# Kernel tuning notes

Measured on AMD Instinct MI355X. Metric: run time of the kernel, lower is better.

## Reference

```python
import jax, jax.numpy as jnp
import numpy as np

NH = 12
RD = 16  # partial RoPE dim


def setup_inputs() -> dict:
    key = jax.random.key(0)
    k1, k2, k3 = jax.random.split(key, 3)
    B, T, C = 4, 2048, 768
    x = jax.random.normal(k1, (B, T, C), dtype=jnp.float32)
    w_qkv = jax.random.normal(k2, (3 * C, C), dtype=jnp.float32) * 0.02
    w_out = jax.random.normal(k3, (C, C), dtype=jnp.float32) * 0.02
    return {"x": x, "w_qkv": w_qkv, "w_out": w_out}


def _rope_tables(T, dtype):
    freqs = 1.0 / (10000.0 ** (jnp.arange(0, RD, 2, dtype=jnp.float32) / RD))
    f = jnp.arange(T, dtype=jnp.float32)[:, None] * freqs[None, :]  # [T, RD//2]
    cos = jnp.cos(f)[None, None].astype(dtype)  # [1,1,T,RD//2]
    sin = jnp.sin(f)[None, None].astype(dtype)
    return cos, sin


def _rope(t, cos, sin):
    # t: [B, H, T, hd]; rotate only the first RD dims (split-half style)
    r, p = t[..., :RD], t[..., RD:]
    r1, r2 = r[..., : RD // 2], r[..., RD // 2 :]
    rot = jnp.concatenate([r1 * cos - r2 * sin, r2 * cos + r1 * sin], axis=-1)
    return jnp.concatenate([rot, p], axis=-1)


def reference(x, w_qkv, w_out):
    B, T, C = x.shape
    hd = C // NH
    qkv = jnp.einsum('btc,dc->btd', x, w_qkv).reshape(B, T, 3, NH, hd)
    q, k, v = (jnp.transpose(qkv[:, :, i], (0, 2, 1, 3)) for i in range(3))  # [B,H,T,hd]
    cos, sin = _rope_tables(T, x.dtype)
    q = _rope(q, cos, sin)
    k = _rope(k, cos, sin)
    scale = 1.0 / np.sqrt(hd).astype(np.float32)
    scores = jnp.einsum('bhqd,bhkd->bhqk', q, k) * scale  # [B,H,T,T]
    causal = jnp.tril(jnp.ones((T, T), dtype=bool))
    scores = jnp.where(causal[None, None], scores, jnp.finfo(scores.dtype).min)
    attn = jax.nn.softmax(scores, axis=-1)
    o = jnp.einsum('bhqk,bhkd->bhqd', attn, v)  # [B,H,T,hd]
    o = jnp.transpose(o, (0, 2, 1, 3)).reshape(B, T, C)
    return jnp.einsum('btc,dc->btd', o, w_out)
```

## Files before the change

kernel.cpp:

```cpp
#include <hip/hip_runtime.h>
#include <math.h>


namespace {

constexpr int B_ = 4, T_ = 2048, C_ = 768, NH_ = 12, HD_ = 64;
constexpr int BH_ = B_ * NH_;
constexpr size_t QS_ = (size_t)BH_ * T_ * HD_;

typedef short short8 __attribute__((ext_vector_type(8)));
typedef float f32x4 __attribute__((ext_vector_type(4)));

__device__ inline ushort f2bf(float f) {
    unsigned u = __builtin_bit_cast(unsigned, f);
    u += 0x7fff + ((u >> 16) & 1);
    return (ushort)(u >> 16);
}
__device__ inline float bf2f(ushort h) {
    unsigned u = (unsigned)h << 16;
    return __builtin_bit_cast(float, u);
}

__global__ __launch_bounds__(256) void cvt_all(
    const float4* __restrict__ x, const float4* __restrict__ wq,
    const float4* __restrict__ wo, ushort4* __restrict__ xb,
    ushort4* __restrict__ wqb, ushort4* __restrict__ wob)
{
    int i = blockIdx.x * 256 + threadIdx.x;
    const float4* s; ushort4* d;
    if (i < 1572864) { s = x; d = xb; }
    else if (i < 2015232) { s = wq; d = wqb; i -= 1572864; }
    else { s = wo; d = wob; i -= 2015232; if (i >= 147456) return; }
    const float4 v = s[i];
    ushort4 u;
    u.x = f2bf(v.x); u.y = f2bf(v.y); u.z = f2bf(v.z); u.w = f2bf(v.w);
    d[i] = u;
}

template <int EPI>
__global__ __launch_bounds__(256) void mgemm(
    const ushort* __restrict__ A, const ushort* __restrict__ Bw,
    float* __restrict__ out, int K, int N_,
    ushort* __restrict__ qb, ushort* __restrict__ kb, ushort* __restrict__ vb)
{
    constexpr int BM = 128, BN = 128, BK = 32;
    __shared__ ushort As[BM * BK];
    __shared__ ushort Bs[BN * BK];

    const int tid = threadIdx.x;
    const int w = tid >> 6, l = tid & 63;
    const int lg = l >> 4, lc = l & 15;
    const int wr = w >> 1, wc = w & 1;
    const int m0 = blockIdx.y * BM;
    const int n0 = blockIdx.x * BN;

    f32x4 acc[4][4] = {};

    for (int k0 = 0; k0 < K; k0 += BK) {
#pragma unroll
        for (int i = 0; i < 2; ++i) {
            const int cb = w * 128 + i * 64;
            const int c = cb + l;
            const ushort* ga = &A[(size_t)(m0 + (c >> 2)) * K + k0 + (c & 3) * 8];
            const ushort* gb = &Bw[(size_t)(n0 + (c >> 2)) * K + k0 + (c & 3) * 8];
            __builtin_amdgcn_global_load_lds(
                (const __attribute__((address_space(1))) void*)ga,
                (__attribute__((address_space(3))) void*)&As[(size_t)cb * 8], 16, 0, 0);
            __builtin_amdgcn_global_load_lds(
                (const __attribute__((address_space(1))) void*)gb,
                (__attribute__((address_space(3))) void*)&Bs[(size_t)cb * 8], 16, 0, 0);
        }
        __syncthreads();

        short8 af[4], bf[4];
#pragma unroll
        for (int mi = 0; mi < 4; ++mi)
            af[mi] = *(const short8*)&As[(wr * 64 + mi * 16 + lc) * 32 + lg * 8];
#pragma unroll
        for (int nj = 0; nj < 4; ++nj)
            bf[nj] = *(const short8*)&Bs[(wc * 64 + nj * 16 + lc) * 32 + lg * 8];
#pragma unroll
        for (int mi = 0; mi < 4; ++mi)
#pragma unroll
            for (int nj = 0; nj < 4; ++nj)
                acc[mi][nj] = __builtin_amdgcn_mfma_f32_16x16x32_bf16(
                    af[mi], bf[nj], acc[mi][nj], 0, 0, 0);
        __syncthreads();
    }

    if constexpr (EPI == 0) {
        (void)qb; (void)kb; (void)vb;
#pragma unroll
        for (int mi = 0; mi < 4; ++mi) {
            const int m = m0 + wr * 64 + mi * 16 + lg * 4;
#pragma unroll
            for (int nj = 0; nj < 4; ++nj) {
                const int n = n0 + wc * 64 + nj * 16 + lc;
#pragma unroll
                for (int r = 0; r < 4; ++r)
                    out[(size_t)(m + r) * N_ + n] = acc[mi][nj][r];
            }
        }
    } else {
        (void)out; (void)N_;
#pragma unroll
        for (int mi = 0; mi < 4; ++mi) {
            const int m = m0 + wr * 64 + mi * 16 + lg * 4;
            const int b = m >> 11, t0 = m & (T_ - 1);
#pragma unroll
            for (int nj = 0; nj < 4; ++nj) {
                const int n = n0 + wc * 64 + nj * 16 + lc;
                const int sec = n / C_;
                const int cc = n - sec * C_;
                const int h = cc >> 6, di = cc & 63;
                if (sec == 2) {
                    ushort4 w4;
                    w4.x = f2bf(acc[mi][nj][0]); w4.y = f2bf(acc[mi][nj][1]);
                    w4.z = f2bf(acc[mi][nj][2]); w4.w = f2bf(acc[mi][nj][3]);
                    *(ushort4*)&vb[((size_t)(b * NH_ + h) * HD_ + di) * T_ + t0] = w4;
                } else {
                    ushort* dst = (sec == 0) ? qb : kb;
                    const float s = (sec == 0) ? 0.18033688f : 1.f;
#pragma unroll
                    for (int r = 0; r < 4; ++r)
                        dst[((size_t)(b * NH_ + h) * T_ + t0 + r) * HD_ + di] =
                            f2bf(acc[mi][nj][r] * s);
                }
            }
        }
    }
}

__global__ __launch_bounds__(256) void rope_kernel(ushort* __restrict__ q,
                                                   ushort* __restrict__ k)
{
    const int g = blockIdx.x * 256 + threadIdx.x;
    const int i = g & 7;
    int row = g >> 3;
    ushort* buf = q;
    if (row >= BH_ * T_) { buf = k; row -= BH_ * T_; }
    const int t = row & (T_ - 1);
    const float freq = __expf(-(float)i * 1.15129254649702f);
    const float a = (float)t * freq;
    const float c = cosf(a), s = sinf(a);
    ushort* p = buf + (size_t)row * HD_;
    const float r1 = bf2f(p[i]), r2 = bf2f(p[i + 8]);
    p[i]     = f2bf(r1 * c - r2 * s);
    p[i + 8] = f2bf(r2 * c + r1 * s);
}

__global__ __launch_bounds__(256) void flash_mfma(
    const ushort* __restrict__ q, const ushort* __restrict__ k,
    const ushort* __restrict__ v, ushort* __restrict__ o)
{
    __shared__ ushort Ks[2][64 * 64];
    __shared__ ushort Vs[2][64 * 64];
    __shared__ ushort Ps[4][16 * 64];

    const int j = blockIdx.x;
    const int bh = blockIdx.y;
    const int b = bh / NH_, h = bh % NH_;
    const int tid = threadIdx.x;
    const int w = tid >> 6, l = tid & 63;
    const int lg = l >> 4, lc = l & 15;

    const size_t kvbase = (size_t)bh * T_ * HD_;
    const size_t vbase  = (size_t)bh * HD_ * T_;

    auto stage = [&](int buf, int t0) {
#pragma unroll
        for (int i = 0; i < 2; ++i) {
            const int cb = (w * 2 + i) * 64;
            const int c = cb + l;
            const int row = c >> 3, s8 = (c & 7) * 8;
            const int col = s8 ^ ((row & 7) << 3);
            __builtin_amdgcn_global_load_lds(
                (const __attribute__((address_space(1))) void*)
                    &k[kvbase + (size_t)(t0 + row) * HD_ + col],
                (__attribute__((address_space(3))) void*)&Ks[buf][cb * 8], 16, 0, 0);
            __builtin_amdgcn_global_load_lds(
                (const __attribute__((address_space(1))) void*)
                    &v[vbase + (size_t)row * T_ + t0 + col],
                (__attribute__((address_space(3))) void*)&Vs[buf][cb * 8], 16, 0, 0);
        }
    };

    int cur = 0;
    stage(0, 0);

    for (int seg = 0; seg < 2; ++seg) {
        const int qi = seg ? (31 - j) : j;
        const int q0 = qi * 64;

        short8 aq[2];
        {
            const ushort* qp =
                q + kvbase + (size_t)(q0 + w * 16 + lc) * HD_ + lg * 8;
            aq[0] = *(const short8*)(qp);
            aq[1] = *(const short8*)(qp + 32);
        }
        f32x4 oa[4] = {};
        float m[4], lr[4];
#pragma unroll
        for (int r = 0; r < 4; ++r) { m[r] = -1e30f; lr[r] = 0.f; }

        const int nkt = qi + 1;
        for (int t0i = 0; t0i < nkt; ++t0i) {
            const int t0 = t0i * 64;
            __syncthreads();
            const bool lastAll = (seg == 1) && (t0i == nkt - 1);
            if (!lastAll) {
                const int nt0 = (t0i + 1 < nkt) ? (t0 + 64) : 0;
                stage(cur ^ 1, nt0);
            }

            f32x4 sa[4];
            __builtin_amdgcn_s_setprio(1);
#pragma unroll
            for (int kc = 0; kc < 4; ++kc) {
                const int row = kc * 16 + lc;
                const int base = row * 64;
                const int sw = (row & 7) << 3;
                short8 b0 = *(const short8*)&Ks[cur][(base + lg * 8) ^ sw];
                short8 b1 = *(const short8*)&Ks[cur][(base + 32 + lg * 8) ^ sw];
                f32x4 z = {0.f, 0.f, 0.f, 0.f};
                z = __builtin_amdgcn_mfma_f32_16x16x32_bf16(aq[0], b0, z, 0, 0, 0);
                z = __builtin_amdgcn_mfma_f32_16x16x32_bf16(aq[1], b1, z, 0, 0, 0);
                sa[kc] = z;
            }
            __builtin_amdgcn_s_setprio(0);

            if (t0 + 63 > q0 + w * 16) {
#pragma unroll
                for (int kc = 0; kc < 4; ++kc) {
                    const int kg = t0 + kc * 16 + lc;
#pragma unroll
                    for (int r = 0; r < 4; ++r) {
                        const int qg = q0 + w * 16 + lg * 4 + r;
                        if (kg > qg) sa[kc][r] = -1e30f;
                    }
                }
            }

            float sc[4];
#pragma unroll
            for (int r = 0; r < 4; ++r) {
                float a = fmaxf(fmaxf(sa[0][r], sa[1][r]),
                                fmaxf(sa[2][r], sa[3][r]));
                a = fmaxf(a, __shfl_xor(a, 1));
                a = fmaxf(a, __shfl_xor(a, 2));
                a = fmaxf(a, __shfl_xor(a, 4));
                a = fmaxf(a, __shfl_xor(a, 8));
                const float mn = fmaxf(m[r], a);
                sc[r] = exp2f(m[r] - mn);
                m[r] = mn;
            }
#pragma unroll
            for (int r = 0; r < 4; ++r) {
                lr[r] *= sc[r];
                oa[0][r] *= sc[r]; oa[1][r] *= sc[r];
                oa[2][r] *= sc[r]; oa[3][r] *= sc[r];
            }
            float ls[4] = {0.f, 0.f, 0.f, 0.f};
#pragma unroll
            for (int kc = 0; kc < 4; ++kc) {
#pragma unroll
                for (int r = 0; r < 4; ++r) {
                    const float p = exp2f(sa[kc][r] - m[r]);
                    ls[r] += p;
                    const int qr = lg * 4 + r;
                    Ps[w][(qr * 64 + kc * 16 + lc) ^ ((qr & 7) << 3)] = f2bf(p);
                }
            }
#pragma unroll
            for (int r = 0; r < 4; ++r) {
                float a = ls[r];
                a += __shfl_xor(a, 1); a += __shfl_xor(a, 2);
                a += __shfl_xor(a, 4); a += __shfl_xor(a, 8);
                lr[r] += a;
            }

            short8 pa[2];
            {
                const int sw = (lc & 7) << 3;
                pa[0] = *(const short8*)&Ps[w][(lc * 64 + lg * 8) ^ sw];
                pa[1] = *(const short8*)&Ps[w][(lc * 64 + 32 + lg * 8) ^ sw];
            }
            __builtin_amdgcn_s_setprio(1);
#pragma unroll
            for (int dc = 0; dc < 4; ++dc) {
                const int row = dc * 16 + lc;
                const int base = row * 64;
                const int sw = (row & 7) << 3;
                short8 b0 = *(const short8*)&Vs[cur][(base + lg * 8) ^ sw];
                short8 b1 = *(const short8*)&Vs[cur][(base + 32 + lg * 8) ^ sw];
                oa[dc] = __builtin_amdgcn_mfma_f32_16x16x32_bf16(pa[0], b0, oa[dc], 0, 0, 0);
                oa[dc] = __builtin_amdgcn_mfma_f32_16x16x32_bf16(pa[1], b1, oa[dc], 0, 0, 0);
            }
            __builtin_amdgcn_s_setprio(0);
            cur ^= 1;
        }

#pragma unroll
        for (int r = 0; r < 4; ++r) {
            const float inv = 1.f / lr[r];
            const int qg = q0 + w * 16 + lg * 4 + r;
            ushort* op = o + (size_t)(b * T_ + qg) * C_ + h * HD_ + lc;
#pragma unroll
            for (int dc = 0; dc < 4; ++dc) op[dc * 16] = f2bf(oa[dc][r] * inv);
        }
    }
}

}

extern "C" void kernel_launch(void* const* d_in, const int* in_sizes, int n_in,
                              void* d_out, int out_size, void* d_ws, size_t ws_size,
                              hipStream_t stream)
{
    (void)in_sizes; (void)n_in; (void)out_size; (void)ws_size;
    const float* x     = (const float*)d_in[0];
    const float* w_qkv = (const float*)d_in[1];
    const float* w_out = (const float*)d_in[2];
    float* out = (float*)d_out;

    ushort* xb    = (ushort*)d_ws;
    ushort* wqkvb = xb + QS_;
    ushort* woutb = wqkvb + (size_t)3 * C_ * C_;
    ushort* qb    = woutb + (size_t)C_ * C_;
    ushort* kb    = qb + QS_;
    ushort* vb    = kb + QS_;
    ushort* ob    = vb + QS_;

    cvt_all<<<8448, 256, 0, stream>>>((const float4*)x, (const float4*)w_qkv,
                                      (const float4*)w_out, (ushort4*)xb,
                                      (ushort4*)wqkvb, (ushort4*)woutb);

    mgemm<1><<<dim3(18, 64), 256, 0, stream>>>(xb, wqkvb, nullptr, C_, 0, qb, kb, vb);

    rope_kernel<<<6144, 256, 0, stream>>>(qb, kb);

    flash_mfma<<<dim3(16, BH_), 256, 0, stream>>>(qb, kb, vb, ob);

    mgemm<0><<<dim3(6, 64), 256, 0, stream>>>(ob, woutb, out, C_, C_,
                                              nullptr, nullptr, nullptr);
}
```

Baseline: 262.1 us.

## Fuse RoPE into QKV GEMM epilogue and add lazy softmax rescaling

Applies partial RoPE inside the QKV GEMM epilogue, exchanging rotation partners with a lane shuffle, so the separate rope kernel and its extra read/write pass over Q and K are removed. In the flash kernel, the running max is only updated and the accumulators rescaled when some row's tile max exceeds the current max by more than a threshold, checked wave-wide. The per-tile row-sum reduction is deferred to the end, and f2bf now uses the library bf16 conversion. Lazy rescaling lets exponent values grow up to 2^8 before renormalising, and starting the max at zero changes the numerics slightly.

Result: faster. 246.1 us (-6.1%).

```diff
diff --git a/kernel.cpp b/kernel.cpp
--- a/kernel.cpp
+++ b/kernel.cpp
@@ -1,4 +1,5 @@
 #include <hip/hip_runtime.h>
+#include <hip/hip_bf16.h>
 #include <math.h>
 
 
@@ -12,13 +13,7 @@
 typedef float f32x4 __attribute__((ext_vector_type(4)));
 
 __device__ inline ushort f2bf(float f) {
-    unsigned u = __builtin_bit_cast(unsigned, f);
-    u += 0x7fff + ((u >> 16) & 1);
-    return (ushort)(u >> 16);
-}
-__device__ inline float bf2f(ushort h) {
-    unsigned u = (unsigned)h << 16;
-    return __builtin_bit_cast(float, u);
+    return __builtin_bit_cast(ushort, __float2bfloat16(f));
 }
 
 __global__ __launch_bounds__(256) void cvt_all(
@@ -120,33 +115,30 @@
                     *(ushort4*)&vb[((size_t)(b * NH_ + h) * HD_ + di) * T_ + t0] = w4;
                 } else {
                     ushort* dst = (sec == 0) ? qb : kb;
-                    const float s = (sec == 0) ? 0.18033688f : 1.f;
+                    const float sfac = (sec == 0) ? 0.18033688f : 1.f;
+                    float vals[4];
+#pragma unroll
+                    for (int r = 0; r < 4; ++r) vals[r] = acc[mi][nj][r] * sfac;
+                    if (di < 16) {
+                        const float fr =
+                            __expf(-(float)(lc & 7) * 1.15129254649702f);
+#pragma unroll
+                        for (int r = 0; r < 4; ++r) {
+                            const float part = __shfl_xor(vals[r], 8);
+                            const float ang = (float)(t0 + r) * fr;
+                            const float cs = cosf(ang), sn = sinf(ang);
+                            vals[r] = (di < 8) ? vals[r] * cs - part * sn
+                                               : vals[r] * cs + part * sn;
+                        }
+                    }
 #pragma unroll
                     for (int r = 0; r < 4; ++r)
                         dst[((size_t)(b * NH_ + h) * T_ + t0 + r) * HD_ + di] =
-                            f2bf(acc[mi][nj][r] * s);
+                            f2bf(vals[r]);
                 }
             }
         }
     }
-}
-
-__global__ __launch_bounds__(256) void rope_kernel(ushort* __restrict__ q,
-                                                   ushort* __restrict__ k)
-{
-    const int g = blockIdx.x * 256 + threadIdx.x;
-    const int i = g & 7;
-    int row = g >> 3;
-    ushort* buf = q;
-    if (row >= BH_ * T_) { buf = k; row -= BH_ * T_; }
-    const int t = row & (T_ - 1);
-    const float freq = __expf(-(float)i * 1.15129254649702f);
-    const float a = (float)t * freq;
-    const float c = cosf(a), s = sinf(a);
-    ushort* p = buf + (size_t)row * HD_;
-    const float r1 = bf2f(p[i]), r2 = bf2f(p[i + 8]);
-    p[i]     = f2bf(r1 * c - r2 * s);
-    p[i + 8] = f2bf(r2 * c + r1 * s);
 }
 
 __global__ __launch_bounds__(256) void flash_mfma(
@@ -200,9 +192,8 @@
             aq[1] = *(const short8*)(qp + 32);
         }
         f32x4 oa[4] = {};
-        float m[4], lr[4];
-#pragma unroll
-        for (int r = 0; r < 4; ++r) { m[r] = -1e30f; lr[r] = 0.f; }
+        float m[4] = {0.f, 0.f, 0.f, 0.f};
+        float lr[4] = {0.f, 0.f, 0.f, 0.f};
 
         const int nkt = qi + 1;
         for (int t0i = 0; t0i < nkt; ++t0i) {
@@ -242,42 +233,39 @@
                 }
             }
 
-            float sc[4];
-#pragma unroll
-            for (int r = 0; r < 4; ++r) {
-                float a = fmaxf(fmaxf(sa[0][r], sa[1][r]),
-                                fmaxf(sa[2][r], sa[3][r]));
-                a = fmaxf(a, __shfl_xor(a, 1));
-                a = fmaxf(a, __shfl_xor(a, 2));
-                a = fmaxf(a, __shfl_xor(a, 4));
-                a = fmaxf(a, __shfl_xor(a, 8));
-                const float mn = fmaxf(m[r], a);
-                sc[r] = exp2f(m[r] - mn);
-                m[r] = mn;
-            }
-#pragma unroll
-            for (int r = 0; r < 4; ++r) {
-                lr[r] *= sc[r];
-                oa[0][r] *= sc[r]; oa[1][r] *= sc[r];
-                oa[2][r] *= sc[r]; oa[3][r] *= sc[r];
-            }
-            float ls[4] = {0.f, 0.f, 0.f, 0.f};
+            float pr[4];
+#pragma unroll
+            for (int r = 0; r < 4; ++r)
+                pr[r] = fmaxf(fmaxf(sa[0][r], sa[1][r]),
+                              fmaxf(sa[2][r], sa[3][r]));
+            const bool ok = (pr[0] <= m[0] + 8.f) & (pr[1] <= m[1] + 8.f) &
+                            (pr[2] <= m[2] + 8.f) & (pr[3] <= m[3] + 8.f);
+            if (!__all(ok)) {
+#pragma unroll
+                for (int r = 0; r < 4; ++r) {
+                    float a = pr[r];
+                    a = fmaxf(a, __shfl_xor(a, 1));
+                    a = fmaxf(a, __shfl_xor(a, 2));
+                    a = fmaxf(a, __shfl_xor(a, 4));
+                    a = fmaxf(a, __shfl_xor(a, 8));
+                    const float mn = fmaxf(m[r], a);
+                    const float sc = exp2f(m[r] - mn);
+                    lr[r] *= sc;
+                    oa[0][r] *= sc; oa[1][r] *= sc;
+                    oa[2][r] *= sc; oa[3][r] *= sc;
+                    m[r] = mn;
+                }
+            }
+
 #pragma unroll
             for (int kc = 0; kc < 4; ++kc) {
 #pragma unroll
                 for (int r = 0; r < 4; ++r) {
                     const float p = exp2f(sa[kc][r] - m[r]);
-                    ls[r] += p;
+                    lr[r] += p;
                     const int qr = lg * 4 + r;
                     Ps[w][(qr * 64 + kc * 16 + lc) ^ ((qr & 7) << 3)] = f2bf(p);
                 }
-            }
-#pragma unroll
-            for (int r = 0; r < 4; ++r) {
-                float a = ls[r];
-                a += __shfl_xor(a, 1); a += __shfl_xor(a, 2);
-                a += __shfl_xor(a, 4); a += __shfl_xor(a, 8);
-                lr[r] += a;
             }
 
             short8 pa[2];
@@ -303,7 +291,10 @@
 
 #pragma unroll
         for (int r = 0; r < 4; ++r) {
-            const float inv = 1.f / lr[r];
+            float a = lr[r];
+            a += __shfl_xor(a, 1); a += __shfl_xor(a, 2);
+            a += __shfl_xor(a, 4); a += __shfl_xor(a, 8);
+            const float inv = 1.f / a;
             const int qg = q0 + w * 16 + lg * 4 + r;
             ushort* op = o + (size_t)(b * T_ + qg) * C_ + h * HD_ + lc;
 #pragma unroll
@@ -338,8 +329,6 @@
 
     mgemm<1><<<dim3(18, 64), 256, 0, stream>>>(xb, wqkvb, nullptr, C_, 0, qb, kb, vb);
 
-    rope_kernel<<<6144, 256, 0, stream>>>(qb, kb);
-
     flash_mfma<<<dim3(16, BH_), 256, 0, stream>>>(qb, kb, vb, ob);
 
     mgemm<0><<<dim3(6, 64), 256, 0, stream>>>(ob, woutb, out, C_, C_,
```
